# Optimization experiments

Measured on AMD Instinct MI355X. Metric: run time of the kernel, lower is better.

## Reference

```python
import jax, jax.numpy as jnp
import numpy as np
import math

EMBED_DIM = 1024
WINDOW = 512


def setup_inputs() -> dict:
    key = jax.random.key(0)
    k_x, k_mb, k_wg, k_bg = jax.random.split(key, 4)
    x = jax.random.normal(k_x, (4, 4096, EMBED_DIM), dtype=jnp.float32)
    memory_bank = jax.random.normal(k_mb, (WINDOW, EMBED_DIM), dtype=jnp.float32)
    # memory_gate: nn.Linear(embed_dim, embed_dim)
    lim = 1.0 / math.sqrt(EMBED_DIM)
    gate_w = jax.random.uniform(k_wg, (EMBED_DIM, EMBED_DIM), jnp.float32, -lim, lim)
    gate_b = jax.random.uniform(k_bg, (EMBED_DIM,), jnp.float32, -lim, lim)
    return {"x": x, "memory_bank": memory_bank, "gate_w": gate_w, "gate_b": gate_b}


def reference(x, memory_bank, gate_w, gate_b):
    d = x.shape[-1]
    # attention scores over fixed memory bank: [B, S, W]
    scores = jnp.einsum("bsd,wd->bsw", x, memory_bank) / jnp.sqrt(jnp.asarray(d, x.dtype))
    attn = jax.nn.softmax(scores, axis=-1)
    retrieved = jnp.einsum("bsw,wd->bsd", attn, memory_bank)
    gate = jax.nn.sigmoid(jnp.einsum("bsd,ed->bse", x, gate_w) + gate_b)
    return gate * x + (1.0 - gate) * retrieved
```

## Files before the change

### kernel.cpp

```cpp
#include <hip/hip_runtime.h>
#include <hip/hip_bf16.h>

#define EMBED 1024
#define WINDOW 512
#define NROWS 16384

typedef __attribute__((ext_vector_type(4))) float f32x4;
typedef __bf16 bf16x8 __attribute__((ext_vector_type(8)));

#define GLDS(g, l)                                                        \
  __builtin_amdgcn_global_load_lds(                                       \
      (const __attribute__((address_space(1))) void*)(const void*)(g),    \
      (__attribute__((address_space(3))) void*)(void*)(l), 16, 0, 0)

__global__ __launch_bounds__(256) void cast_bf16_kernel(
    const float* __restrict__ in, __bf16* __restrict__ out, int n8) {
  int i = blockIdx.x * blockDim.x + threadIdx.x;
  if (i >= n8) return;
  const f32x4* p = (const f32x4*)(in + (size_t)i * 8);
  f32x4 a = p[0], b = p[1];
  bf16x8 o = {(__bf16)a[0], (__bf16)a[1], (__bf16)a[2], (__bf16)a[3],
              (__bf16)b[0], (__bf16)b[1], (__bf16)b[2], (__bf16)b[3]};
  *(bf16x8*)(out + (size_t)i * 8) = o;
}

__global__ __launch_bounds__(256) void transpose_mb_lds_kernel(
    const float* __restrict__ mb, __bf16* __restrict__ mbt) {
  __shared__ __bf16 tile[32][33];
  const int tx = threadIdx.x & 7, ty = threadIdx.x >> 3;
  const int w0 = (blockIdx.x & 15) * 32;
  const int d0 = (blockIdx.x >> 4) * 32;
  f32x4 v = *(const f32x4*)(mb + (size_t)(w0 + ty) * EMBED + d0 + tx * 4);
#pragma unroll
  for (int j = 0; j < 4; ++j) tile[tx * 4 + j][ty] = (__bf16)v[j];
  __syncthreads();
  unsigned u0 =
      ((unsigned)__builtin_bit_cast(unsigned short, tile[ty][tx * 4 + 1]) << 16) |
      (unsigned)__builtin_bit_cast(unsigned short, tile[ty][tx * 4 + 0]);
  unsigned u1 =
      ((unsigned)__builtin_bit_cast(unsigned short, tile[ty][tx * 4 + 3]) << 16) |
      (unsigned)__builtin_bit_cast(unsigned short, tile[ty][tx * 4 + 2]);
  uint2 w2 = {u0, u1};
  *(uint2*)(mbt + (size_t)(d0 + ty) * WINDOW + w0 + tx * 4) = w2;
}

__global__ __launch_bounds__(256) void softmax_kernel(__bf16* __restrict__ s1) {
  const int row = blockIdx.x * 4 + (threadIdx.x >> 6);
  const int lane = threadIdx.x & 63;
  __bf16* p = s1 + (size_t)row * WINDOW + lane * 8;
  bf16x8 v = *(const bf16x8*)p;
  float f[8];
  float mx = -1e30f;
#pragma unroll
  for (int j = 0; j < 8; ++j) {
    f[j] = (float)v[j] * 0.03125f;
    mx = fmaxf(mx, f[j]);
  }
#pragma unroll
  for (int off = 1; off < 64; off <<= 1) mx = fmaxf(mx, __shfl_xor(mx, off));
  float s = 0.f;
#pragma unroll
  for (int j = 0; j < 8; ++j) {
    f[j] = __expf(f[j] - mx);
    s += f[j];
  }
#pragma unroll
  for (int off = 1; off < 64; off <<= 1) s += __shfl_xor(s, off);
  const float inv = 1.0f / s;
  bf16x8 o;
#pragma unroll
  for (int j = 0; j < 8; ++j) o[j] = (__bf16)(f[j] * inv);
  *(bf16x8*)p = o;
}

#define SLOADFRAGS(cb, kk)                                                    \
  {                                                                           \
    const __bf16* As_ = &ldsA[cb][(warp_m * 64 + fr) * 64];                   \
    const __bf16* Bs_ = &ldsB[cb][(warp_n * 64 + fr) * 64];                   \
    const int pg_ = (((kk)*4 + fq) ^ (fr & 7)) * 8;                           \
    _Pragma("unroll") for (int m = 0; m < 4; ++m)                             \
        af[m] = *(const bf16x8*)(As_ + m * 16 * 64 + pg_);                    \
    _Pragma("unroll") for (int n = 0; n < 4; ++n)                             \
        bfv[n] = *(const bf16x8*)(Bs_ + n * 16 * 64 + pg_);                   \
  }

#define SMFMA16(ACC)                                                          \
  {                                                                           \
    __builtin_amdgcn_s_barrier();                                             \
    asm volatile("s_waitcnt lgkmcnt(0)" ::: "memory");                        \
    __builtin_amdgcn_s_setprio(1);                                            \
    _Pragma("unroll") for (int m = 0; m < 4; ++m)                             \
        _Pragma("unroll") for (int n = 0; n < 4; ++n)                         \
            ACC[m][n] = __builtin_amdgcn_mfma_f32_16x16x32_bf16(              \
                af[m], bfv[n], ACC[m][n], 0, 0, 0);                           \
    __builtin_amdgcn_s_setprio(0);                                            \
    __builtin_amdgcn_s_barrier();                                             \
  }

__global__ __launch_bounds__(512, 2) void gemm_scores_kernel(
    const __bf16* __restrict__ xb, const __bf16* __restrict__ mbb,
    __bf16* __restrict__ s1) {
  __shared__ __align__(16) __bf16 ldsA[3][256 * 64];
  __shared__ __align__(16) __bf16 ldsB[3][128 * 64];
  const int tid = threadIdx.x;
  const int lane = tid & 63;
  const int wave = tid >> 6;
  const int bid = blockIdx.x;
  const int xcd = bid & 7;
  const int idx = bid >> 3;
  const int bm = xcd * 8 + (idx & 7);
  const int bn = idx >> 3;
  const int row0 = bm * 256;
  const int col0 = bn * 128;
  const int warp_m = wave >> 1;
  const int warp_n = wave & 1;
  const int srow = lane >> 3;
  const int sgc = (lane & 7) ^ srow;
  const int wv32 = wave * 32;
  const int wv16 = wave * 16;
  const int fr = lane & 15;
  const int fq = lane >> 4;

  const __bf16* aS = xb + (size_t)(row0 + wv32 + srow) * EMBED + sgc * 8;
  const __bf16* bS = mbb + (size_t)(col0 + wv16 + srow) * EMBED + sgc * 8;

#define STAGE_S1(vt, buf)                                                     \
  {                                                                           \
    const int k0_ = (vt)*64;                                                  \
    _Pragma("unroll") for (int c = 0; c < 2; ++c)                             \
        GLDS(aS + (size_t)c * 8 * EMBED + k0_, &ldsA[buf][(wv32 + c * 8) * 64]); \
    GLDS(bS + k0_, &ldsB[buf][wv16 * 64]);                                    \
  }
#define STAGE_S2(vt, buf)                                                     \
  {                                                                           \
    const int k0_ = (vt)*64;                                                  \
    _Pragma("unroll") for (int c = 2; c < 4; ++c)                             \
        GLDS(aS + (size_t)c * 8 * EMBED + k0_, &ldsA[buf][(wv32 + c * 8) * 64]); \
    GLDS(bS + (size_t)8 * EMBED + k0_, &ldsB[buf][(wv16 + 8) * 64]);          \
  }

  f32x4 acc[4][4];
#pragma unroll
  for (int m = 0; m < 4; ++m)
#pragma unroll
    for (int n = 0; n < 4; ++n) acc[m][n] = (f32x4){0.f, 0.f, 0.f, 0.f};
  bf16x8 af[4], bfv[4];

  STAGE_S1(0, 0); STAGE_S2(0, 0);
  STAGE_S1(1, 1); STAGE_S2(1, 1);
  asm volatile("s_waitcnt vmcnt(6)" ::: "memory");
  __builtin_amdgcn_s_barrier();

  const int NT = 16;
  for (int vt = 0; vt < NT; ++vt) {
    const int cb = vt % 3;
    const int nb = (vt + 2) % 3;
    SLOADFRAGS(cb, 0);
    if (vt + 2 < NT) STAGE_S1(vt + 2, nb);
    SMFMA16(acc);
    SLOADFRAGS(cb, 1);
    if (vt + 2 < NT) STAGE_S2(vt + 2, nb);
    if (vt < NT - 2) {
      asm volatile("s_waitcnt vmcnt(6)" ::: "memory");
    } else if (vt == NT - 2) {
      asm volatile("s_waitcnt vmcnt(0)" ::: "memory");
    }
    SMFMA16(acc);
  }
#undef STAGE_S1
#undef STAGE_S2

#pragma unroll
  for (int n = 0; n < 4; ++n) {
    const int col = col0 + warp_n * 64 + n * 16 + fr;
#pragma unroll
    for (int m = 0; m < 4; ++m)
#pragma unroll
      for (int j = 0; j < 4; ++j) {
        const int row = row0 + warp_m * 64 + m * 16 + fq * 4 + j;
        s1[(size_t)row * WINDOW + col] = (__bf16)acc[m][n][j];
      }
  }
}

__global__ __launch_bounds__(256, 2) void dual_fused128_kernel(
    const __bf16* __restrict__ s1, const __bf16* __restrict__ xb,
    const __bf16* __restrict__ mbt, const __bf16* __restrict__ gwb,
    const float* __restrict__ gb, float* __restrict__ out) {
  __shared__ __align__(16) __bf16 ldsA[2][128 * 64];
  __shared__ __align__(16) __bf16 ldsB[2][128 * 64];
  const int tid = threadIdx.x, lane = tid & 63, wave = tid >> 6;
  const int bid = blockIdx.x;
  const int xcd = bid & 7;
  const int g = bid >> 3;
  const int bm = xcd * 16 + (g >> 3);
  const int bn = g & 7;
  const int row0 = bm * 128, col0 = bn * 128;
  const int warp_m = wave >> 1, warp_n = wave & 1;
  const int fr = lane & 15, fq = lane >> 4;
  const int srow = lane >> 3;
  const int sgc = (lane & 7) ^ srow;
  const int wv32 = wave * 32;

  const __bf16* aR = s1 + (size_t)(row0 + wv32 + srow) * WINDOW + sgc * 8;
  const __bf16* bR = mbt + (size_t)(col0 + wv32 + srow) * WINDOW + sgc * 8;
  const __bf16* aG = xb + (size_t)(row0 + wv32 + srow) * EMBED + sgc * 8;
  const __bf16* bG = gwb + (size_t)(col0 + wv32 + srow) * EMBED + sgc * 8;

#define STG(vt, buf)                                                          \
  {                                                                           \
    if ((vt) < 8) {                                                           \
      const int k0_ = (vt)*64;                                                \
      _Pragma("unroll") for (int c = 0; c < 4; ++c)                           \
          GLDS(aR + (size_t)c * 8 * WINDOW + k0_,                             \
               &ldsA[buf][(wv32 + c * 8) * 64]);                              \
      _Pragma("unroll") for (int c = 0; c < 4; ++c)                           \
          GLDS(bR + (size_t)c * 8 * WINDOW + k0_,                             \
               &ldsB[buf][(wv32 + c * 8) * 64]);                              \
    } else {                                                                  \
      const int k0_ = ((vt)-8) * 64;                                          \
      _Pragma("unroll") for (int c = 0; c < 4; ++c)                           \
          GLDS(aG + (size_t)c * 8 * EMBED + k0_,                              \
               &ldsA[buf][(wv32 + c * 8) * 64]);                              \
      _Pragma("unroll") for (int c = 0; c < 4; ++c)                           \
          GLDS(bG + (size_t)c * 8 * EMBED + k0_,                              \
               &ldsB[buf][(wv32 + c * 8) * 64]);                              \
    }                                                                         \
  }

#define BARF                                                                  \
  {                                                                           \
    asm volatile("" ::: "memory");                                            \
    __builtin_amdgcn_s_barrier();                                             \
    asm volatile("" ::: "memory");                                            \
  }

#define COMPUTE(ACC, cur)                                                     \
  {                                                                           \
    const __bf16* As_ = &ldsA[cur][(warp_m * 64 + fr) * 64];                  \
    const __bf16* Bs_ = &ldsB[cur][(warp_n * 64 + fr) * 64];                  \
    _Pragma("unroll") for (int kk = 0; kk < 2; ++kk) {                        \
      const int pg_ = ((kk * 4 + fq) ^ (fr & 7)) * 8;                         \
      bf16x8 af[4], bfv[4];                                                   \
      _Pragma("unroll") for (int m = 0; m < 4; ++m)                           \
          af[m] = *(const bf16x8*)(As_ + m * 16 * 64 + pg_);                  \
      _Pragma("unroll") for (int n = 0; n < 4; ++n)                           \
          bfv[n] = *(const bf16x8*)(Bs_ + n * 16 * 64 + pg_);                 \
      __builtin_amdgcn_s_setprio(1);                                          \
      _Pragma("unroll") for (int m = 0; m < 4; ++m)                           \
          _Pragma("unroll") for (int n = 0; n < 4; ++n)                       \
              ACC[m][n] = __builtin_amdgcn_mfma_f32_16x16x32_bf16(            \
                  af[m], bfv[n], ACC[m][n], 0, 0, 0);                         \
      __builtin_amdgcn_s_setprio(0);                                          \
    }                                                                         \
  }

  f32x4 accr[4][4], accg[4][4];
#pragma unroll
  for (int m = 0; m < 4; ++m)
#pragma unroll
    for (int n = 0; n < 4; ++n) {
      accr[m][n] = (f32x4){0.f, 0.f, 0.f, 0.f};
      accg[m][n] = (f32x4){0.f, 0.f, 0.f, 0.f};
    }

  STG(0, 0);
  for (int vt = 0; vt < 8; ++vt) {
    const int cur = vt & 1;
    STG(vt + 1, cur ^ 1);
    asm volatile("s_waitcnt vmcnt(8)" ::: "memory");
    BARF;
    COMPUTE(accr, cur);
    BARF;
  }
  for (int vt = 8; vt < 24; ++vt) {
    const int cur = vt & 1;
    if (vt + 1 < 24) {
      STG(vt + 1, cur ^ 1);
      asm volatile("s_waitcnt vmcnt(8)" ::: "memory");
    } else {
      asm volatile("s_waitcnt vmcnt(0)" ::: "memory");
    }
    BARF;
    COMPUTE(accg, cur);
    BARF;
  }
#undef STG
#undef COMPUTE
#undef BARF

#pragma unroll
  for (int n = 0; n < 4; ++n) {
    const int col = col0 + warp_n * 64 + n * 16 + fr;
    const float bias = gb[col];
#pragma unroll
    for (int m = 0; m < 4; ++m) {
#pragma unroll
      for (int j = 0; j < 4; ++j) {
        const int row = row0 + warp_m * 64 + m * 16 + fq * 4 + j;
        const size_t o = (size_t)row * EMBED + col;
        const float gt = 1.0f / (1.0f + __expf(-(accg[m][n][j] + bias)));
        const float xv = (float)xb[o];
        out[o] = gt * xv + (1.0f - gt) * accr[m][n][j];
      }
    }
  }
}

extern "C" void kernel_launch(void* const* d_in, const int* in_sizes, int n_in,
                              void* d_out, int out_size, void* d_ws,
                              size_t ws_size, hipStream_t stream) {
  const float* x = (const float*)d_in[0];
  const float* mb = (const float*)d_in[1];
  const float* gw = (const float*)d_in[2];
  const float* gb = (const float*)d_in[3];
  float* out = (float*)d_out;

  char* ws = (char*)d_ws;
  __bf16* xb = (__bf16*)(ws);
  __bf16* mbb = (__bf16*)(ws + 33554432);
  __bf16* mbt = (__bf16*)(ws + 34603008);
  __bf16* gwb = (__bf16*)(ws + 35651584);
  __bf16* s1 = (__bf16*)(ws + 37748736);

  cast_bf16_kernel<<<8192, 256, 0, stream>>>(x, xb, 2097152);
  cast_bf16_kernel<<<256, 256, 0, stream>>>(mb, mbb, 65536);
  cast_bf16_kernel<<<512, 256, 0, stream>>>(gw, gwb, 131072);
  transpose_mb_lds_kernel<<<512, 256, 0, stream>>>(mb, mbt);
  gemm_scores_kernel<<<256, 512, 0, stream>>>(xb, mbb, s1);
  softmax_kernel<<<4096, 256, 0, stream>>>(s1);
  dual_fused128_kernel<<<1024, 256, 0, stream>>>(s1, xb, mbt, gwb, gb, out);
}
```

Before: 117.1 us.

## Fuse fp32-to-bf16 cast of x into GEMM loads and split retrieval GEMM

Removes the standalone cast of x to bf16. The scores and gate GEMMs now load fp32 x through registers, pack it to bf16 and write it into swizzled LDS, with B staged by async global-to-LDS loads. The former dual fused kernel is split in two: a retrieval GEMM that writes bf16 retrieved values to the workspace, and a gate GEMM whose epilogue reads fp32 x and the retrieved tile. This avoids writing and re-reading a 32MB bf16 copy of x, but x is now read in fp32 twice, and there is an extra bf16 intermediate plus an extra launch.

```diff
diff --git a/kernel.cpp b/kernel.cpp
--- a/kernel.cpp
+++ b/kernel.cpp
@@ -12,6 +12,10 @@
   __builtin_amdgcn_global_load_lds(                                       \
       (const __attribute__((address_space(1))) void*)(const void*)(g),    \
       (__attribute__((address_space(3))) void*)(void*)(l), 16, 0, 0)
+
+static __device__ __forceinline__ unsigned bfb(float v) {
+  return (unsigned)__builtin_bit_cast(unsigned short, (__bf16)v);
+}
 
 __global__ __launch_bounds__(256) void cast_bf16_kernel(
     const float* __restrict__ in, __bf16* __restrict__ out, int n8) {
@@ -34,12 +38,10 @@
 #pragma unroll
   for (int j = 0; j < 4; ++j) tile[tx * 4 + j][ty] = (__bf16)v[j];
   __syncthreads();
-  unsigned u0 =
-      ((unsigned)__builtin_bit_cast(unsigned short, tile[ty][tx * 4 + 1]) << 16) |
-      (unsigned)__builtin_bit_cast(unsigned short, tile[ty][tx * 4 + 0]);
-  unsigned u1 =
-      ((unsigned)__builtin_bit_cast(unsigned short, tile[ty][tx * 4 + 3]) << 16) |
-      (unsigned)__builtin_bit_cast(unsigned short, tile[ty][tx * 4 + 2]);
+  unsigned u0 = (bfb((float)tile[ty][tx * 4 + 1]) << 16) |
+                bfb((float)tile[ty][tx * 4 + 0]);
+  unsigned u1 = (bfb((float)tile[ty][tx * 4 + 3]) << 16) |
+                bfb((float)tile[ty][tx * 4 + 2]);
   uint2 w2 = {u0, u1};
   *(uint2*)(mbt + (size_t)(d0 + ty) * WINDOW + w0 + tx * 4) = w2;
 }
@@ -73,33 +75,158 @@
   *(bf16x8*)p = o;
 }
 
-#define SLOADFRAGS(cb, kk)                                                    \
-  {                                                                           \
-    const __bf16* As_ = &ldsA[cb][(warp_m * 64 + fr) * 64];                   \
-    const __bf16* Bs_ = &ldsB[cb][(warp_n * 64 + fr) * 64];                   \
-    const int pg_ = (((kk)*4 + fq) ^ (fr & 7)) * 8;                           \
-    _Pragma("unroll") for (int m = 0; m < 4; ++m)                             \
-        af[m] = *(const bf16x8*)(As_ + m * 16 * 64 + pg_);                    \
-    _Pragma("unroll") for (int n = 0; n < 4; ++n)                             \
-        bfv[n] = *(const bf16x8*)(Bs_ + n * 16 * 64 + pg_);                   \
-  }
-
-#define SMFMA16(ACC)                                                          \
-  {                                                                           \
+template <int EPI, int NBN>
+__global__ __launch_bounds__(512, 1) void gemm_xA_kernel(
+    const float* __restrict__ x, const __bf16* __restrict__ bmat,
+    __bf16* __restrict__ s1out, const __bf16* __restrict__ rbb,
+    const float* __restrict__ gb, float* __restrict__ out) {
+  __shared__ __align__(16) __bf16 ldsA[2][256 * 64];
+  __shared__ __align__(16) __bf16 ldsB[3][128 * 64];
+  const int tid = threadIdx.x, lane = tid & 63, wave = tid >> 6;
+  const int bid = blockIdx.x;
+  const int xcd = bid & 7;
+  const int g = bid >> 3;
+  const int bn = g & (NBN - 1);
+  const int bm = xcd * 8 + (g >> (NBN == 4 ? 2 : 3));
+  const int row0 = bm * 256, col0 = bn * 128;
+  const int warp_m = wave >> 1, warp_n = wave & 1;
+  const int fr = lane & 15, fq = lane >> 4;
+
+  const int arow = tid >> 1;
+  const int ahalf = tid & 1;
+  const float* aSrc = x + (size_t)(row0 + arow) * EMBED + ahalf * 32;
+
+  const int srow = lane >> 3;
+  const int sgc = (lane & 7) ^ srow;
+  const int wv16 = wave * 16;
+  const __bf16* bS = bmat + (size_t)(col0 + wv16 + srow) * EMBED + sgc * 8;
+
+#define ALOAD(dst, t)                                                         \
+  {                                                                           \
+    _Pragma("unroll") for (int j = 0; j < 8; ++j)                             \
+        dst[j] = *(const f32x4*)(aSrc + (t) * 64 + j * 4);                    \
+    asm volatile("" ::: "memory");                                            \
+  }
+#define STG_B(t, slot)                                                        \
+  {                                                                           \
+    GLDS(bS + (t) * 64, &ldsB[slot][wv16 * 64]);                              \
+    GLDS(bS + (size_t)8 * EMBED + (t) * 64, &ldsB[slot][(wv16 + 8) * 64]);    \
+  }
+#define APACK(src, buf)                                                       \
+  {                                                                           \
+    _Pragma("unroll") for (int gi = 0; gi < 4; ++gi) {                        \
+      uint4 w;                                                                \
+      w.x = (bfb(src[2 * gi][1]) << 16) | bfb(src[2 * gi][0]);                \
+      w.y = (bfb(src[2 * gi][3]) << 16) | bfb(src[2 * gi][2]);                \
+      w.z = (bfb(src[2 * gi + 1][1]) << 16) | bfb(src[2 * gi + 1][0]);        \
+      w.w = (bfb(src[2 * gi + 1][3]) << 16) | bfb(src[2 * gi + 1][2]);        \
+      *(uint4*)(&ldsA[buf][arow * 64 +                                        \
+                           (((ahalf * 4 + gi) ^ (arow & 7)) * 8)]) = w;       \
+    }                                                                         \
+  }
+#define XCOMPUTE(cur, bslot)                                                  \
+  {                                                                           \
+    const __bf16* As_ = &ldsA[cur][(warp_m * 64 + fr) * 64];                  \
+    const __bf16* Bs_ = &ldsB[bslot][(warp_n * 64 + fr) * 64];                \
+    _Pragma("unroll") for (int kk = 0; kk < 2; ++kk) {                        \
+      const int pg_ = ((kk * 4 + fq) ^ (fr & 7)) * 8;                         \
+      bf16x8 af[4], bfv[4];                                                   \
+      _Pragma("unroll") for (int m = 0; m < 4; ++m)                           \
+          af[m] = *(const bf16x8*)(As_ + m * 16 * 64 + pg_);                  \
+      _Pragma("unroll") for (int n = 0; n < 4; ++n)                           \
+          bfv[n] = *(const bf16x8*)(Bs_ + n * 16 * 64 + pg_);                 \
+      __builtin_amdgcn_s_setprio(1);                                          \
+      _Pragma("unroll") for (int m = 0; m < 4; ++m)                           \
+          _Pragma("unroll") for (int n = 0; n < 4; ++n)                       \
+              acc[m][n] = __builtin_amdgcn_mfma_f32_16x16x32_bf16(            \
+                  af[m], bfv[n], acc[m][n], 0, 0, 0);                         \
+      __builtin_amdgcn_s_setprio(0);                                          \
+    }                                                                         \
+  }
+#define BARX                                                                  \
+  {                                                                           \
+    asm volatile("" ::: "memory");                                            \
     __builtin_amdgcn_s_barrier();                                             \
-    asm volatile("s_waitcnt lgkmcnt(0)" ::: "memory");                        \
-    __builtin_amdgcn_s_setprio(1);                                            \
-    _Pragma("unroll") for (int m = 0; m < 4; ++m)                             \
-        _Pragma("unroll") for (int n = 0; n < 4; ++n)                         \
-            ACC[m][n] = __builtin_amdgcn_mfma_f32_16x16x32_bf16(              \
-                af[m], bfv[n], ACC[m][n], 0, 0, 0);                           \
-    __builtin_amdgcn_s_setprio(0);                                            \
-    __builtin_amdgcn_s_barrier();                                             \
-  }
-
-__global__ __launch_bounds__(512, 2) void gemm_scores_kernel(
-    const __bf16* __restrict__ xb, const __bf16* __restrict__ mbb,
-    __bf16* __restrict__ s1) {
+    asm volatile("" ::: "memory");                                            \
+  }
+#define TBODY(t, PK, LD)                                                      \
+  {                                                                           \
+    if ((t) + 3 < NT) ALOAD(LD, (t) + 3);                                     \
+    if ((t) + 2 < NT) STG_B((t) + 2, ((t) + 2) % 3);                          \
+    XCOMPUTE((t) & 1, (t) % 3);                                               \
+    BARX;                                                                     \
+    if ((t) + 3 < NT) {                                                       \
+      asm volatile("s_waitcnt vmcnt(10)" ::: "memory");                       \
+    } else if ((t) + 2 < NT) {                                                \
+      asm volatile("s_waitcnt vmcnt(2)" ::: "memory");                        \
+    } else if ((t) + 1 < NT) {                                                \
+      asm volatile("s_waitcnt vmcnt(0)" ::: "memory");                        \
+    }                                                                         \
+    if ((t) + 2 < NT) {                                                       \
+      APACK(PK, (t) & 1);                                                     \
+      asm volatile("s_waitcnt lgkmcnt(0)" ::: "memory");                      \
+    }                                                                         \
+    BARX;                                                                     \
+  }
+
+  f32x4 acc[4][4];
+#pragma unroll
+  for (int m = 0; m < 4; ++m)
+#pragma unroll
+    for (int n = 0; n < 4; ++n) acc[m][n] = (f32x4){0.f, 0.f, 0.f, 0.f};
+
+  const int NT = 16;
+  f32x4 av[8], nv[8];
+  ALOAD(av, 0);
+  STG_B(0, 0);
+  asm volatile("s_waitcnt vmcnt(2)" ::: "memory");
+  APACK(av, 0);
+  ALOAD(av, 1);
+  STG_B(1, 1);
+  asm volatile("s_waitcnt vmcnt(2)" ::: "memory");
+  APACK(av, 1);
+  ALOAD(av, 2);
+  asm volatile("s_waitcnt lgkmcnt(0)" ::: "memory");
+  __builtin_amdgcn_s_barrier();
+
+  for (int t = 0; t < NT; t += 2) {
+    TBODY(t, av, nv);
+    TBODY(t + 1, nv, av);
+  }
+#undef TBODY
+#undef BARX
+#undef XCOMPUTE
+#undef APACK
+#undef STG_B
+#undef ALOAD
+
+#pragma unroll
+  for (int n = 0; n < 4; ++n) {
+    const int col = col0 + warp_n * 64 + n * 16 + fr;
+    float bias = 0.f;
+    if (EPI == 1) bias = gb[col];
+#pragma unroll
+    for (int m = 0; m < 4; ++m) {
+#pragma unroll
+      for (int j = 0; j < 4; ++j) {
+        const int row = row0 + warp_m * 64 + m * 16 + fq * 4 + j;
+        if (EPI == 0) {
+          s1out[(size_t)row * WINDOW + col] = (__bf16)acc[m][n][j];
+        } else {
+          const size_t o = (size_t)row * EMBED + col;
+          const float gt = 1.0f / (1.0f + __expf(-(acc[m][n][j] + bias)));
+          const float xv = x[o];
+          const float rv = (float)rbb[o];
+          out[o] = gt * xv + (1.0f - gt) * rv;
+        }
+      }
+    }
+  }
+}
+
+__global__ __launch_bounds__(512, 1) void gemm_retr_kernel(
+    const __bf16* __restrict__ s1, const __bf16* __restrict__ mbt,
+    __bf16* __restrict__ rbb) {
   __shared__ __align__(16) __bf16 ldsA[3][256 * 64];
   __shared__ __align__(16) __bf16 ldsB[3][128 * 64];
   const int tid = threadIdx.x;
@@ -107,9 +234,9 @@
   const int wave = tid >> 6;
   const int bid = blockIdx.x;
   const int xcd = bid & 7;
-  const int idx = bid >> 3;
-  const int bm = xcd * 8 + (idx & 7);
-  const int bn = idx >> 3;
+  const int g = bid >> 3;
+  const int bm = xcd * 8 + (g >> 3);
+  const int bn = g & 7;
   const int row0 = bm * 256;
   const int col0 = bn * 128;
   const int warp_m = wave >> 1;
@@ -121,22 +248,46 @@
   const int fr = lane & 15;
   const int fq = lane >> 4;
 
-  const __bf16* aS = xb + (size_t)(row0 + wv32 + srow) * EMBED + sgc * 8;
-  const __bf16* bS = mbb + (size_t)(col0 + wv16 + srow) * EMBED + sgc * 8;
-
-#define STAGE_S1(vt, buf)                                                     \
+  const __bf16* aS = s1 + (size_t)(row0 + wv32 + srow) * WINDOW + sgc * 8;
+  const __bf16* bS = mbt + (size_t)(col0 + wv16 + srow) * WINDOW + sgc * 8;
+
+#define STAGE_R1(vt, buf)                                                     \
   {                                                                           \
     const int k0_ = (vt)*64;                                                  \
     _Pragma("unroll") for (int c = 0; c < 2; ++c)                             \
-        GLDS(aS + (size_t)c * 8 * EMBED + k0_, &ldsA[buf][(wv32 + c * 8) * 64]); \
+        GLDS(aS + (size_t)c * 8 * WINDOW + k0_,                               \
+             &ldsA[buf][(wv32 + c * 8) * 64]);                                \
     GLDS(bS + k0_, &ldsB[buf][wv16 * 64]);                                    \
   }
-#define STAGE_S2(vt, buf)                                                     \
+#define STAGE_R2(vt, buf)                                                     \
   {                                                                           \
     const int k0_ = (vt)*64;                                                  \
     _Pragma("unroll") for (int c = 2; c < 4; ++c)                             \
-        GLDS(aS + (size_t)c * 8 * EMBED + k0_, &ldsA[buf][(wv32 + c * 8) * 64]); \
-    GLDS(bS + (size_t)8 * EMBED + k0_, &ldsB[buf][(wv16 + 8) * 64]);          \
+        GLDS(aS + (size_t)c * 8 * WINDOW + k0_,                               \
+             &ldsA[buf][(wv32 + c * 8) * 64]);                                \
+    GLDS(bS + (size_t)8 * WINDOW + k0_, &ldsB[buf][(wv16 + 8) * 64]);         \
+  }
+#define RLOADFRAGS(cb, kk)                                                    \
+  {                                                                           \
+    const __bf16* As_ = &ldsA[cb][(warp_m * 64 + fr) * 64];                   \
+    const __bf16* Bs_ = &ldsB[cb][(warp_n * 64 + fr) * 64];                   \
+    const int pg_ = (((kk)*4 + fq) ^ (fr & 7)) * 8;                           \
+    _Pragma("unroll") for (int m = 0; m < 4; ++m)                             \
+        af[m] = *(const bf16x8*)(As_ + m * 16 * 64 + pg_);                    \
+    _Pragma("unroll") for (int n = 0; n < 4; ++n)                             \
+        bfv[n] = *(const bf16x8*)(Bs_ + n * 16 * 64 + pg_);                   \
+  }
+#define RMFMA16                                                               \
+  {                                                                           \
+    __builtin_amdgcn_s_barrier();                                             \
+    asm volatile("s_waitcnt lgkmcnt(0)" ::: "memory");                        \
+    __builtin_amdgcn_s_setprio(1);                                            \
+    _Pragma("unroll") for (int m = 0; m < 4; ++m)                             \
+        _Pragma("unroll") for (int n = 0; n < 4; ++n)                         \
+            acc[m][n] = __builtin_amdgcn_mfma_f32_16x16x32_bf16(              \
+                af[m], bfv[n], acc[m][n], 0, 0, 0);                           \
+    __builtin_amdgcn_s_setprio(0);                                            \
+    __builtin_amdgcn_s_barrier();                                             \
   }
 
   f32x4 acc[4][4];
@@ -146,29 +297,31 @@
     for (int n = 0; n < 4; ++n) acc[m][n] = (f32x4){0.f, 0.f, 0.f, 0.f};
   bf16x8 af[4], bfv[4];
 
-  STAGE_S1(0, 0); STAGE_S2(0, 0);
-  STAGE_S1(1, 1); STAGE_S2(1, 1);
+  STAGE_R1(0, 0); STAGE_R2(0, 0);
+  STAGE_R1(1, 1); STAGE_R2(1, 1);
   asm volatile("s_waitcnt vmcnt(6)" ::: "memory");
   __builtin_amdgcn_s_barrier();
 
-  const int NT = 16;
+  const int NT = 8;
   for (int vt = 0; vt < NT; ++vt) {
     const int cb = vt % 3;
     const int nb = (vt + 2) % 3;
-    SLOADFRAGS(cb, 0);
-    if (vt + 2 < NT) STAGE_S1(vt + 2, nb);
-    SMFMA16(acc);
-    SLOADFRAGS(cb, 1);
-    if (vt + 2 < NT) STAGE_S2(vt + 2, nb);
+    RLOADFRAGS(cb, 0);
+    if (vt + 2 < NT) STAGE_R1(vt + 2, nb);
+    RMFMA16;
+    RLOADFRAGS(cb, 1);
+    if (vt + 2 < NT) STAGE_R2(vt + 2, nb);
     if (vt < NT - 2) {
       asm volatile("s_waitcnt vmcnt(6)" ::: "memory");
     } else if (vt == NT - 2) {
       asm volatile("s_waitcnt vmcnt(0)" ::: "memory");
     }
-    SMFMA16(acc);
-  }
-#undef STAGE_S1
-#undef STAGE_S2
+    RMFMA16;
+  }
+#undef STAGE_R1
+#undef STAGE_R2
+#undef RLOADFRAGS
+#undef RMFMA16
 
 #pragma unroll
   for (int n = 0; n < 4; ++n) {
@@ -178,132 +331,8 @@
 #pragma unroll
       for (int j = 0; j < 4; ++j) {
         const int row = row0 + warp_m * 64 + m * 16 + fq * 4 + j;
-        s1[(size_t)row * WINDOW + col] = (__bf16)acc[m][n][j];
+        rbb[(size_t)row * EMBED + col] = (__bf16)acc[m][n][j];
       }
-  }
-}
-
-__global__ __launch_bounds__(256, 2) void dual_fused128_kernel(
-    const __bf16* __restrict__ s1, const __bf16* __restrict__ xb,
-    const __bf16* __restrict__ mbt, const __bf16* __restrict__ gwb,
-    const float* __restrict__ gb, float* __restrict__ out) {
-  __shared__ __align__(16) __bf16 ldsA[2][128 * 64];
-  __shared__ __align__(16) __bf16 ldsB[2][128 * 64];
-  const int tid = threadIdx.x, lane = tid & 63, wave = tid >> 6;
-  const int bid = blockIdx.x;
-  const int xcd = bid & 7;
-  const int g = bid >> 3;
-  const int bm = xcd * 16 + (g >> 3);
-  const int bn = g & 7;
-  const int row0 = bm * 128, col0 = bn * 128;
-  const int warp_m = wave >> 1, warp_n = wave & 1;
-  const int fr = lane & 15, fq = lane >> 4;
-  const int srow = lane >> 3;
-  const int sgc = (lane & 7) ^ srow;
-  const int wv32 = wave * 32;
-
-  const __bf16* aR = s1 + (size_t)(row0 + wv32 + srow) * WINDOW + sgc * 8;
-  const __bf16* bR = mbt + (size_t)(col0 + wv32 + srow) * WINDOW + sgc * 8;
-  const __bf16* aG = xb + (size_t)(row0 + wv32 + srow) * EMBED + sgc * 8;
-  const __bf16* bG = gwb + (size_t)(col0 + wv32 + srow) * EMBED + sgc * 8;
-
-#define STG(vt, buf)                                                          \
-  {                                                                           \
-    if ((vt) < 8) {                                                           \
-      const int k0_ = (vt)*64;                                                \
-      _Pragma("unroll") for (int c = 0; c < 4; ++c)                           \
-          GLDS(aR + (size_t)c * 8 * WINDOW + k0_,                             \
-               &ldsA[buf][(wv32 + c * 8) * 64]);                              \
-      _Pragma("unroll") for (int c = 0; c < 4; ++c)                           \
-          GLDS(bR + (size_t)c * 8 * WINDOW + k0_,                             \
-               &ldsB[buf][(wv32 + c * 8) * 64]);                              \
-    } else {                                                                  \
-      const int k0_ = ((vt)-8) * 64;                                          \
-      _Pragma("unroll") for (int c = 0; c < 4; ++c)                           \
-          GLDS(aG + (size_t)c * 8 * EMBED + k0_,                              \
-               &ldsA[buf][(wv32 + c * 8) * 64]);                              \
-      _Pragma("unroll") for (int c = 0; c < 4; ++c)                           \
-          GLDS(bG + (size_t)c * 8 * EMBED + k0_,                              \
-               &ldsB[buf][(wv32 + c * 8) * 64]);                              \
-    }                                                                         \
-  }
-
-#define BARF                                                                  \
-  {                                                                           \
-    asm volatile("" ::: "memory");                                            \
-    __builtin_amdgcn_s_barrier();                                             \
-    asm volatile("" ::: "memory");                                            \
-  }
-
-#define COMPUTE(ACC, cur)                                                     \
-  {                                                                           \
-    const __bf16* As_ = &ldsA[cur][(warp_m * 64 + fr) * 64];                  \
-    const __bf16* Bs_ = &ldsB[cur][(warp_n * 64 + fr) * 64];                  \
-    _Pragma("unroll") for (int kk = 0; kk < 2; ++kk) {                        \
-      const int pg_ = ((kk * 4 + fq) ^ (fr & 7)) * 8;                         \
-      bf16x8 af[4], bfv[4];                                                   \
-      _Pragma("unroll") for (int m = 0; m < 4; ++m)                           \
-          af[m] = *(const bf16x8*)(As_ + m * 16 * 64 + pg_);                  \
-      _Pragma("unroll") for (int n = 0; n < 4; ++n)                           \
-          bfv[n] = *(const bf16x8*)(Bs_ + n * 16 * 64 + pg_);                 \
-      __builtin_amdgcn_s_setprio(1);                                          \
-      _Pragma("unroll") for (int m = 0; m < 4; ++m)                           \
-          _Pragma("unroll") for (int n = 0; n < 4; ++n)                       \
-              ACC[m][n] = __builtin_amdgcn_mfma_f32_16x16x32_bf16(            \
-                  af[m], bfv[n], ACC[m][n], 0, 0, 0);                         \
-      __builtin_amdgcn_s_setprio(0);                                          \
-    }                                                                         \
-  }
-
-  f32x4 accr[4][4], accg[4][4];
-#pragma unroll
-  for (int m = 0; m < 4; ++m)
-#pragma unroll
-    for (int n = 0; n < 4; ++n) {
-      accr[m][n] = (f32x4){0.f, 0.f, 0.f, 0.f};
-      accg[m][n] = (f32x4){0.f, 0.f, 0.f, 0.f};
-    }
-
-  STG(0, 0);
-  for (int vt = 0; vt < 8; ++vt) {
-    const int cur = vt & 1;
-    STG(vt + 1, cur ^ 1);
-    asm volatile("s_waitcnt vmcnt(8)" ::: "memory");
-    BARF;
-    COMPUTE(accr, cur);
-    BARF;
-  }
-  for (int vt = 8; vt < 24; ++vt) {
-    const int cur = vt & 1;
-    if (vt + 1 < 24) {
-      STG(vt + 1, cur ^ 1);
-      asm volatile("s_waitcnt vmcnt(8)" ::: "memory");
-    } else {
-      asm volatile("s_waitcnt vmcnt(0)" ::: "memory");
-    }
-    BARF;
-    COMPUTE(accg, cur);
-    BARF;
-  }
-#undef STG
-#undef COMPUTE
-#undef BARF
-
-#pragma unroll
-  for (int n = 0; n < 4; ++n) {
-    const int col = col0 + warp_n * 64 + n * 16 + fr;
-    const float bias = gb[col];
-#pragma unroll
-    for (int m = 0; m < 4; ++m) {
-#pragma unroll
-      for (int j = 0; j < 4; ++j) {
-        const int row = row0 + warp_m * 64 + m * 16 + fq * 4 + j;
-        const size_t o = (size_t)row * EMBED + col;
-        const float gt = 1.0f / (1.0f + __expf(-(accg[m][n][j] + bias)));
-        const float xv = (float)xb[o];
-        out[o] = gt * xv + (1.0f - gt) * accr[m][n][j];
-      }
-    }
   }
 }
 
@@ -317,17 +346,17 @@
   float* out = (float*)d_out;
 
   char* ws = (char*)d_ws;
-  __bf16* xb = (__bf16*)(ws);
+  __bf16* rbb = (__bf16*)(ws);
   __bf16* mbb = (__bf16*)(ws + 33554432);
   __bf16* mbt = (__bf16*)(ws + 34603008);
   __bf16* gwb = (__bf16*)(ws + 35651584);
   __bf16* s1 = (__bf16*)(ws + 37748736);
 
-  cast_bf16_kernel<<<8192, 256, 0, stream>>>(x, xb, 2097152);
   cast_bf16_kernel<<<256, 256, 0, stream>>>(mb, mbb, 65536);
   cast_bf16_kernel<<<512, 256, 0, stream>>>(gw, gwb, 131072);
   transpose_mb_lds_kernel<<<512, 256, 0, stream>>>(mb, mbt);
-  gemm_scores_kernel<<<256, 512, 0, stream>>>(xb, mbb, s1);
+  gemm_xA_kernel<0, 4><<<256, 512, 0, stream>>>(x, mbb, s1, nullptr, gb, out);
   softmax_kernel<<<4096, 256, 0, stream>>>(s1);
-  dual_fused128_kernel<<<1024, 256, 0, stream>>>(s1, xb, mbt, gwb, gb, out);
-}
+  gemm_retr_kernel<<<512, 512, 0, stream>>>(s1, mbt, rbb);
+  gemm_xA_kernel<1, 8><<<512, 512, 0, stream>>>(x, gwb, nullptr, rbb, gb, out);
+}
```

New measurement: 197.4 us. 1.69x slower.

## Split fused dual GEMM into two 256x128 pipelined GEMMs via templated kernel

Applied to the files above, without the earlier changes.

Generalizes the scores GEMM into a templated 256x128-tile, triple-buffered kernel. When the workspace is large enough, it replaces the fused 128x128 dual GEMM with two launches: attn@memory_bank written to a bf16 buffer, then x@gate_w with a gate-blend epilogue that reads that buffer. The goal is to reuse the larger-tile, better-pipelined GEMM for both products. The cost is an extra bf16 intermediate write and read plus one more launch. The scores GEMM also changes its block-to-tile mapping.

```diff
diff --git a/kernel.cpp b/kernel.cpp
--- a/kernel.cpp
+++ b/kernel.cpp
@@ -12,6 +12,10 @@
   __builtin_amdgcn_global_load_lds(                                       \
       (const __attribute__((address_space(1))) void*)(const void*)(g),    \
       (__attribute__((address_space(3))) void*)(void*)(l), 16, 0, 0)
+
+static __device__ __forceinline__ unsigned bfb(float v) {
+  return (unsigned)__builtin_bit_cast(unsigned short, (__bf16)v);
+}
 
 __global__ __launch_bounds__(256) void cast_bf16_kernel(
     const float* __restrict__ in, __bf16* __restrict__ out, int n8) {
@@ -34,12 +38,10 @@
 #pragma unroll
   for (int j = 0; j < 4; ++j) tile[tx * 4 + j][ty] = (__bf16)v[j];
   __syncthreads();
-  unsigned u0 =
-      ((unsigned)__builtin_bit_cast(unsigned short, tile[ty][tx * 4 + 1]) << 16) |
-      (unsigned)__builtin_bit_cast(unsigned short, tile[ty][tx * 4 + 0]);
-  unsigned u1 =
-      ((unsigned)__builtin_bit_cast(unsigned short, tile[ty][tx * 4 + 3]) << 16) |
-      (unsigned)__builtin_bit_cast(unsigned short, tile[ty][tx * 4 + 2]);
+  unsigned u0 = (bfb((float)tile[ty][tx * 4 + 1]) << 16) |
+                bfb((float)tile[ty][tx * 4 + 0]);
+  unsigned u1 = (bfb((float)tile[ty][tx * 4 + 3]) << 16) |
+                bfb((float)tile[ty][tx * 4 + 2]);
   uint2 w2 = {u0, u1};
   *(uint2*)(mbt + (size_t)(d0 + ty) * WINDOW + w0 + tx * 4) = w2;
 }
@@ -73,33 +75,12 @@
   *(bf16x8*)p = o;
 }
 
-#define SLOADFRAGS(cb, kk)                                                    \
-  {                                                                           \
-    const __bf16* As_ = &ldsA[cb][(warp_m * 64 + fr) * 64];                   \
-    const __bf16* Bs_ = &ldsB[cb][(warp_n * 64 + fr) * 64];                   \
-    const int pg_ = (((kk)*4 + fq) ^ (fr & 7)) * 8;                           \
-    _Pragma("unroll") for (int m = 0; m < 4; ++m)                             \
-        af[m] = *(const bf16x8*)(As_ + m * 16 * 64 + pg_);                    \
-    _Pragma("unroll") for (int n = 0; n < 4; ++n)                             \
-        bfv[n] = *(const bf16x8*)(Bs_ + n * 16 * 64 + pg_);                   \
-  }
-
-#define SMFMA16(ACC)                                                          \
-  {                                                                           \
-    __builtin_amdgcn_s_barrier();                                             \
-    asm volatile("s_waitcnt lgkmcnt(0)" ::: "memory");                        \
-    __builtin_amdgcn_s_setprio(1);                                            \
-    _Pragma("unroll") for (int m = 0; m < 4; ++m)                             \
-        _Pragma("unroll") for (int n = 0; n < 4; ++n)                         \
-            ACC[m][n] = __builtin_amdgcn_mfma_f32_16x16x32_bf16(              \
-                af[m], bfv[n], ACC[m][n], 0, 0, 0);                           \
-    __builtin_amdgcn_s_setprio(0);                                            \
-    __builtin_amdgcn_s_barrier();                                             \
-  }
-
-__global__ __launch_bounds__(512, 2) void gemm_scores_kernel(
-    const __bf16* __restrict__ xb, const __bf16* __restrict__ mbb,
-    __bf16* __restrict__ s1) {
+template <int NT, int LDA_, int LDB_, int NBN, int EPI, int OSTR>
+__global__ __launch_bounds__(512, 2) void gemm_sp_kernel(
+    const __bf16* __restrict__ A, const __bf16* __restrict__ B,
+    __bf16* __restrict__ outb, const __bf16* __restrict__ xb,
+    const __bf16* __restrict__ rbb, const float* __restrict__ gb,
+    float* __restrict__ out) {
   __shared__ __align__(16) __bf16 ldsA[3][256 * 64];
   __shared__ __align__(16) __bf16 ldsB[3][128 * 64];
   const int tid = threadIdx.x;
@@ -108,8 +89,8 @@
   const int bid = blockIdx.x;
   const int xcd = bid & 7;
   const int idx = bid >> 3;
-  const int bm = xcd * 8 + (idx & 7);
-  const int bn = idx >> 3;
+  const int bn = idx & (NBN - 1);
+  const int bm = xcd * 8 + (idx >> (NBN == 4 ? 2 : 3));
   const int row0 = bm * 256;
   const int col0 = bn * 128;
   const int warp_m = wave >> 1;
@@ -121,22 +102,46 @@
   const int fr = lane & 15;
   const int fq = lane >> 4;
 
-  const __bf16* aS = xb + (size_t)(row0 + wv32 + srow) * EMBED + sgc * 8;
-  const __bf16* bS = mbb + (size_t)(col0 + wv16 + srow) * EMBED + sgc * 8;
-
-#define STAGE_S1(vt, buf)                                                     \
+  const __bf16* aS = A + (size_t)(row0 + wv32 + srow) * LDA_ + sgc * 8;
+  const __bf16* bS = B + (size_t)(col0 + wv16 + srow) * LDB_ + sgc * 8;
+
+#define STAGE_P1(vt, buf)                                                     \
   {                                                                           \
     const int k0_ = (vt)*64;                                                  \
     _Pragma("unroll") for (int c = 0; c < 2; ++c)                             \
-        GLDS(aS + (size_t)c * 8 * EMBED + k0_, &ldsA[buf][(wv32 + c * 8) * 64]); \
+        GLDS(aS + (size_t)c * 8 * LDA_ + k0_,                                 \
+             &ldsA[buf][(wv32 + c * 8) * 64]);                                \
     GLDS(bS + k0_, &ldsB[buf][wv16 * 64]);                                    \
   }
-#define STAGE_S2(vt, buf)                                                     \
+#define STAGE_P2(vt, buf)                                                     \
   {                                                                           \
     const int k0_ = (vt)*64;                                                  \
     _Pragma("unroll") for (int c = 2; c < 4; ++c)                             \
-        GLDS(aS + (size_t)c * 8 * EMBED + k0_, &ldsA[buf][(wv32 + c * 8) * 64]); \
-    GLDS(bS + (size_t)8 * EMBED + k0_, &ldsB[buf][(wv16 + 8) * 64]);          \
+        GLDS(aS + (size_t)c * 8 * LDA_ + k0_,                                 \
+             &ldsA[buf][(wv32 + c * 8) * 64]);                                \
+    GLDS(bS + (size_t)8 * LDB_ + k0_, &ldsB[buf][(wv16 + 8) * 64]);           \
+  }
+#define PLOADFRAGS(cb, kk)                                                    \
+  {                                                                           \
+    const __bf16* As_ = &ldsA[cb][(warp_m * 64 + fr) * 64];                   \
+    const __bf16* Bs_ = &ldsB[cb][(warp_n * 64 + fr) * 64];                   \
+    const int pg_ = (((kk)*4 + fq) ^ (fr & 7)) * 8;                           \
+    _Pragma("unroll") for (int m = 0; m < 4; ++m)                             \
+        af[m] = *(const bf16x8*)(As_ + m * 16 * 64 + pg_);                    \
+    _Pragma("unroll") for (int n = 0; n < 4; ++n)                             \
+        bfv[n] = *(const bf16x8*)(Bs_ + n * 16 * 64 + pg_);                   \
+  }
+#define PMFMA16                                                               \
+  {                                                                           \
+    __builtin_amdgcn_s_barrier();                                             \
+    asm volatile("s_waitcnt lgkmcnt(0)" ::: "memory");                        \
+    __builtin_amdgcn_s_setprio(1);                                            \
+    _Pragma("unroll") for (int m = 0; m < 4; ++m)                             \
+        _Pragma("unroll") for (int n = 0; n < 4; ++n)                         \
+            acc[m][n] = __builtin_amdgcn_mfma_f32_16x16x32_bf16(              \
+                af[m], bfv[n], acc[m][n], 0, 0, 0);                           \
+    __builtin_amdgcn_s_setprio(0);                                            \
+    __builtin_amdgcn_s_barrier();                                             \
   }
 
   f32x4 acc[4][4];
@@ -146,40 +151,50 @@
     for (int n = 0; n < 4; ++n) acc[m][n] = (f32x4){0.f, 0.f, 0.f, 0.f};
   bf16x8 af[4], bfv[4];
 
-  STAGE_S1(0, 0); STAGE_S2(0, 0);
-  STAGE_S1(1, 1); STAGE_S2(1, 1);
+  STAGE_P1(0, 0); STAGE_P2(0, 0);
+  STAGE_P1(1, 1); STAGE_P2(1, 1);
   asm volatile("s_waitcnt vmcnt(6)" ::: "memory");
   __builtin_amdgcn_s_barrier();
 
-  const int NT = 16;
   for (int vt = 0; vt < NT; ++vt) {
     const int cb = vt % 3;
     const int nb = (vt + 2) % 3;
-    SLOADFRAGS(cb, 0);
-    if (vt + 2 < NT) STAGE_S1(vt + 2, nb);
-    SMFMA16(acc);
-    SLOADFRAGS(cb, 1);
-    if (vt + 2 < NT) STAGE_S2(vt + 2, nb);
+    PLOADFRAGS(cb, 0);
+    if (vt + 2 < NT) STAGE_P1(vt + 2, nb);
+    PMFMA16;
+    PLOADFRAGS(cb, 1);
+    if (vt + 2 < NT) STAGE_P2(vt + 2, nb);
     if (vt < NT - 2) {
       asm volatile("s_waitcnt vmcnt(6)" ::: "memory");
     } else if (vt == NT - 2) {
       asm volatile("s_waitcnt vmcnt(0)" ::: "memory");
     }
-    SMFMA16(acc);
-  }
-#undef STAGE_S1
-#undef STAGE_S2
+    PMFMA16;
+  }
+#undef STAGE_P1
+#undef STAGE_P2
+#undef PLOADFRAGS
+#undef PMFMA16
 
 #pragma unroll
   for (int n = 0; n < 4; ++n) {
     const int col = col0 + warp_n * 64 + n * 16 + fr;
-#pragma unroll
-    for (int m = 0; m < 4; ++m)
+    float bias = 0.f;
+    if (EPI == 1) bias = gb[col];
+#pragma unroll
+    for (int m = 0; m < 4; ++m) {
 #pragma unroll
       for (int j = 0; j < 4; ++j) {
         const int row = row0 + warp_m * 64 + m * 16 + fq * 4 + j;
-        s1[(size_t)row * WINDOW + col] = (__bf16)acc[m][n][j];
+        if (EPI == 0) {
+          outb[(size_t)row * OSTR + col] = (__bf16)acc[m][n][j];
+        } else {
+          const size_t o = (size_t)row * EMBED + col;
+          const float gt = 1.0f / (1.0f + __expf(-(acc[m][n][j] + bias)));
+          out[o] = gt * (float)xb[o] + (1.0f - gt) * (float)rbb[o];
+        }
       }
+    }
   }
 }
 
@@ -322,12 +337,22 @@
   __bf16* mbt = (__bf16*)(ws + 34603008);
   __bf16* gwb = (__bf16*)(ws + 35651584);
   __bf16* s1 = (__bf16*)(ws + 37748736);
+  __bf16* rbb = (__bf16*)(ws + 54525952);
+  const bool ws_big = ws_size >= 88080384ull;
 
   cast_bf16_kernel<<<8192, 256, 0, stream>>>(x, xb, 2097152);
   cast_bf16_kernel<<<256, 256, 0, stream>>>(mb, mbb, 65536);
   cast_bf16_kernel<<<512, 256, 0, stream>>>(gw, gwb, 131072);
   transpose_mb_lds_kernel<<<512, 256, 0, stream>>>(mb, mbt);
-  gemm_scores_kernel<<<256, 512, 0, stream>>>(xb, mbb, s1);
+  gemm_sp_kernel<16, EMBED, EMBED, 4, 0, WINDOW><<<256, 512, 0, stream>>>(
+      xb, mbb, s1, nullptr, nullptr, gb, out);
   softmax_kernel<<<4096, 256, 0, stream>>>(s1);
-  dual_fused128_kernel<<<1024, 256, 0, stream>>>(s1, xb, mbt, gwb, gb, out);
-}
+  if (ws_big) {
+    gemm_sp_kernel<8, WINDOW, WINDOW, 8, 0, EMBED><<<512, 512, 0, stream>>>(
+        s1, mbt, rbb, nullptr, nullptr, gb, out);
+    gemm_sp_kernel<16, EMBED, EMBED, 8, 1, EMBED><<<512, 512, 0, stream>>>(
+        xb, gwb, nullptr, xb, rbb, gb, out);
+  } else {
+    dual_fused128_kernel<<<1024, 256, 0, stream>>>(s1, xb, mbt, gwb, gb, out);
+  }
+}
```

New measurement: 133.1 us. +13.7%, slower.
